# Performance work log

Measured on AMD Instinct MI355X. Metric: run time of the kernel, lower is better.

## Reference

```python
import jax, jax.numpy as jnp
import numpy as np

BOX_WARP = 1.0
RAY_START = 2.25
RAY_END = 3.3
S = 32  # depth_resolution (coarse), N_importance = 0


def bilinear_sample(image, coords):
    """Faithful port of the custom grid_sample (align_corners=True mapping).
    image: [B, C, H, W]; coords: [B, M, 2] in [-1, 1]. Returns [B, M, C]."""
    B, C, H, W = image.shape
    ix = (coords[..., 0] + 1.0) * 0.5 * (W - 1)
    iy = (coords[..., 1] + 1.0) * 0.5 * (H - 1)
    ix0 = jnp.floor(ix)
    iy0 = jnp.floor(iy)
    ix1 = ix0 + 1.0
    iy1 = iy0 + 1.0
    # weights use UNclamped corner positions, matching the torch code
    w_nw = (ix1 - ix) * (iy1 - iy)
    w_ne = (ix - ix0) * (iy1 - iy)
    w_sw = (ix1 - ix) * (iy - iy0)
    w_se = (ix - ix0) * (iy - iy0)
    ix0c = jnp.clip(ix0, 0, W - 1).astype(jnp.int32)
    ix1c = jnp.clip(ix1, 0, W - 1).astype(jnp.int32)
    iy0c = jnp.clip(iy0, 0, H - 1).astype(jnp.int32)
    iy1c = jnp.clip(iy1, 0, H - 1).astype(jnp.int32)
    img = image.reshape(B, C, H * W)

    def gather(iyc, ixc):
        idx = iyc * W + ixc  # [B, M]
        return jnp.take_along_axis(img, idx[:, None, :], axis=2)  # [B, C, M]

    out = (gather(iy0c, ix0c) * w_nw[:, None, :]
           + gather(iy0c, ix1c) * w_ne[:, None, :]
           + gather(iy1c, ix0c) * w_sw[:, None, :]
           + gather(iy1c, ix1c) * w_se[:, None, :])
    return out.transpose(0, 2, 1)  # [B, M, C]


def setup_inputs() -> dict:
    key = jax.random.key(0)
    k1, k2, k3, k4, k5 = jax.random.split(key, 5)
    N, n_planes, C, H, W = 2, 3, 32, 256, 256
    R = 16384
    vol_planes = jax.random.normal(k1, (N, n_planes, C, H, W), dtype=jnp.float32)
    dirs = jax.random.normal(k2, (N, R, 3), dtype=jnp.float32)
    dirs = dirs / jnp.linalg.norm(dirs, axis=-1, keepdims=True)
    # camera on sphere of radius 2.7 looking through origin -> samples in box
    ray_origins = -2.7 * dirs
    w1 = jax.random.normal(k3, (C, 64), dtype=jnp.float32) * (1.0 / np.sqrt(C))
    b1 = jnp.zeros((64,), dtype=jnp.float32)
    w2 = jax.random.normal(k4, (64, 33), dtype=jnp.float32) * (1.0 / 8.0)
    b2 = jnp.zeros((33,), dtype=jnp.float32)
    return {"vol_planes": vol_planes, "ray_origins": ray_origins,
            "ray_directions": dirs, "w1": w1, "b1": b1, "w2": w2, "b2": b2}


def reference(vol_planes, ray_origins, ray_directions, w1, b1, w2, b2):
    N, n_planes, C, H, W = vol_planes.shape
    R = ray_origins.shape[1]
    # --- sample_stratified (deterministic: midpoint of each bin) ---
    t = (jnp.arange(S, dtype=vol_planes.dtype) + 0.5) / S
    d = RAY_START + (RAY_END - RAY_START) * t  # [S]
    depths = jnp.broadcast_to(d[None, None, :, None], (N, R, S, 1))
    coords = ray_origins[:, :, None, :] + depths * ray_directions[:, :, None, :]
    M = R * S
    coords = coords.reshape(N, M, 3) * (2.0 / BOX_WARP)
    # --- project_onto_planes (vol_proj=True): xyz, yzx, xzy; sampler uses xy ---
    xy = coords[..., jnp.array([0, 1])]
    yz = coords[..., jnp.array([1, 2])]
    xz = coords[..., jnp.array([0, 2])]
    proj = jnp.stack([xy, yz, xz], axis=1).reshape(N * n_planes, M, 2)
    feats = bilinear_sample(vol_planes.reshape(N * n_planes, C, H, W), proj)
    feats = feats.reshape(N, n_planes, M, C).mean(axis=1)  # aggregate planes
    # --- decoder: small MLP -> 1 sigma + 32 rgb features (EG3D style) ---
    h = jax.nn.softplus(feats @ w1 + b1)
    o = h @ w2 + b2
    sigma = o[..., :1].reshape(N, R, S, 1)
    rgb = (jax.nn.sigmoid(o[..., 1:]) * 1.002 - 0.001).reshape(N, R, S, 32)
    # --- MipRayMarcher2 ---
    deltas = depths[:, :, 1:] - depths[:, :, :-1]
    colors_mid = 0.5 * (rgb[:, :, :-1] + rgb[:, :, 1:])
    densities_mid = 0.5 * (sigma[:, :, :-1] + sigma[:, :, 1:])
    densities_mid = jax.nn.softplus(densities_mid - 1.0)
    alpha = 1.0 - jnp.exp(-deltas * densities_mid)  # [N,R,S-1,1]
    trans = jnp.cumprod(
        jnp.concatenate([jnp.ones_like(alpha[:, :, :1]), 1.0 - alpha + 1e-10],
                        axis=2), axis=2)[:, :, :-1]
    weights = alpha * trans
    rgb_final = (weights * colors_mid).sum(axis=2)  # [N, R, 32]
    return rgb_final
```

## Files before the change

### kernel.cpp

```cpp
#include <hip/hip_runtime.h>
#include <math.h>

#define HH 256
#define WW 256
#define CC 32
#define SS 32
#define NRAYS 32768
#define RPB 8

#define FXB_OFF 0
#define SIG_OFF 20480
#define WST_OFF 21504
#define W2T_OFF 25600
#define ALP_OFF 31744
#define POOLSZ  32768

typedef __attribute__((ext_vector_type(8))) short short8;
typedef __attribute__((ext_vector_type(4))) float f32x4;

__device__ __forceinline__ f32x4 mfma16(short8 a, short8 b, f32x4 c) {
    return __builtin_amdgcn_mfma_f32_16x16x32_bf16(a, b, c, 0, 0, 0);
}

__device__ __forceinline__ float bf2f(unsigned short u) {
    union { unsigned int ui; float f; } v; v.ui = ((unsigned int)u) << 16; return v.f;
}
__device__ __forceinline__ float lo2f(unsigned int w) {
    union { unsigned int ui; float f; } v; v.ui = w << 16; return v.f;
}
__device__ __forceinline__ float hi2f(unsigned int w) {
    union { unsigned int ui; float f; } v; v.ui = w & 0xffff0000u; return v.f;
}
__device__ __forceinline__ unsigned short f2bf(float f) {
    union { float f; unsigned int u; } v; v.f = f;
    unsigned int u = v.u;
    unsigned int r = u + 0x7fffu + ((u >> 16) & 1u);
    return (unsigned short)(r >> 16);
}
__device__ __forceinline__ unsigned int pk_bf16(float a, float b) {
    return (unsigned int)f2bf(a) | ((unsigned int)f2bf(b) << 16);
}
__device__ __forceinline__ int iclamp(int x, int lo, int hi) {
    return x < lo ? lo : (x > hi ? hi : x);
}
__device__ __forceinline__ float softplus_f(float z) {
    return fmaxf(z, 0.f) + log1pf(expf(-fabsf(z)));
}
__device__ __forceinline__ float softplus_fast(float z) {
    return fmaxf(z, 0.f) + __logf(1.0f + __expf(-fabsf(z)));
}
__device__ __forceinline__ float sigmoid_fast(float z) {
    return __builtin_amdgcn_rcpf(1.0f + __expf(-z));
}

template<bool F32>
__device__ __forceinline__ float ldv(const void* p, size_t i) {
    if (F32) return ((const float*)p)[i];
    else     return bf2f(((const unsigned short*)p)[i]);
}

__device__ __forceinline__ int compute_flag(const void* rayo) {
    const float* f = (const float*)rayo;
    const unsigned short* u = (const unsigned short*)rayo;
    float sf = 0.f, sb = 0.f;
    for (int r = 0; r < 8; r++) {
        const float a = f[3 * r], b = f[3 * r + 1], c = f[3 * r + 2];
        sf += fminf(fabsf(a * a + b * b + c * c - 7.29f), 1e3f);
        const float x = bf2f(u[3 * r]), y = bf2f(u[3 * r + 1]), z = bf2f(u[3 * r + 2]);
        sb += fminf(fabsf(x * x + y * y + z * z - 7.29f), 1e3f);
    }
    return (sf < sb) ? 1 : 0;
}

__global__ __launch_bounds__(1024) void transpose_tex(
    const void* __restrict__ vol, unsigned short* __restrict__ tex,
    const void* __restrict__ rayo) {
    __shared__ __align__(16) unsigned short tb[32][129];
    __shared__ int fsh;
    const int l = threadIdx.x;
    if (l == 0) fsh = compute_flag(rayo);
    __syncthreads();
    const int flag = fsh;

    const int tx = l & 31, ty = l >> 5;
    const int wq = l >> 3, cq = l & 7;
    const int w0 = blockIdx.x * 128;
    const int h  = blockIdx.y;
    const int img = blockIdx.z;
    const size_t srcE = (((size_t)img * CC + ty) * HH + h) * WW + w0 + 4 * tx;
    const size_t dstE = (((size_t)img * HH + h) * WW + (w0 + wq)) * CC + 4 * cq;
    if (flag) {
        const float4 v = *(const float4*)((const float*)vol + srcE);
        tb[ty][4 * tx + 0] = f2bf(v.x); tb[ty][4 * tx + 1] = f2bf(v.y);
        tb[ty][4 * tx + 2] = f2bf(v.z); tb[ty][4 * tx + 3] = f2bf(v.w);
    } else {
        *(ushort4*)&tb[ty][4 * tx] = *(const ushort4*)((const unsigned short*)vol + srcE);
    }
    __syncthreads();
    ushort4 o;
    o.x = tb[4 * cq + 0][wq]; o.y = tb[4 * cq + 1][wq];
    o.z = tb[4 * cq + 2][wq]; o.w = tb[4 * cq + 3][wq];
    *(ushort4*)(tex + dstE) = o;
}

template<bool F32>
__device__ void render_mfma_body(
    const unsigned short* __restrict__ tex,
    const void* __restrict__ rayo, const void* __restrict__ rayd,
    const void* __restrict__ w1b, const void* __restrict__ b1b,
    const void* __restrict__ w2b, const void* __restrict__ b2b,
    void* __restrict__ outp, char* __restrict__ pool)
{
    const int t = threadIdx.x;
    unsigned short* fxB = (unsigned short*)(pool + FXB_OFF);
    float* sigL = (float*)(pool + SIG_OFF);
    unsigned short* w1t = (unsigned short*)(pool + WST_OFF);
    unsigned short* w2t = (unsigned short*)(pool + W2T_OFF);
    float* aL = (float*)(pool + ALP_OFF);

    for (int i = t; i < 2048; i += 256) {
        const int n = i >> 5, k = i & 31;
        w1t[i] = f2bf(ldv<F32>(w1b, (size_t)k * 64 + n));
    }
    for (int i = t; i < 3072; i += 256) {
        const int n = i >> 6, k = i & 63;
        w2t[i] = (n < 33) ? f2bf(ldv<F32>(w2b, (size_t)k * 33 + n)) : (unsigned short)0;
    }
    __syncthreads();

    {
        const int rl = t >> 5;
        const int L  = t & 31;
        const int c4 = L & 7;
        const int sub = L >> 3;
        const int gray = blockIdx.x * RPB + rl;
        const int n = gray >> 14;
        const size_t rb = (size_t)gray * 3;
        const float ox = ldv<F32>(rayo, rb), oy = ldv<F32>(rayo, rb + 1), oz = ldv<F32>(rayo, rb + 2);
        const float dx = ldv<F32>(rayd, rb), dy = ldv<F32>(rayd, rb + 1), dz = ldv<F32>(rayd, rb + 2);
        const char* texb = (const char*)tex;
        const unsigned int cb = (unsigned int)c4 * 8;

        #pragma unroll 2
        for (int k = 0; k < 8; ++k) {
            const int s = sub * 8 + k;
            const float d = 2.25f + 1.05f * ((s + 0.5f) * (1.0f / 32.0f));
            const float x = (ox + d * dx) * 2.0f;
            const float y = (oy + d * dy) * 2.0f;
            const float z = (oz + d * dz) * 2.0f;
            float a0[4] = {0.f, 0.f, 0.f, 0.f};
            float a1[4] = {0.f, 0.f, 0.f, 0.f};
            float a2[4] = {0.f, 0.f, 0.f, 0.f};
            #pragma unroll
            for (int p = 0; p < 3; p++) {
                const float u = (p == 0) ? x : ((p == 1) ? y : x);
                const float v = (p == 0) ? y : z;
                const float ixf = fmaf(u, 127.5f, 127.5f);
                const float iyf = fmaf(v, 127.5f, 127.5f);
                const float ix0f = floorf(ixf), iy0f = floorf(iyf);
                const float wx1 = ixf - ix0f, wy1 = iyf - iy0f;
                const float wx0 = 1.f - wx1,  wy0 = 1.f - wy1;
                const int ix0 = iclamp((int)ix0f, 0, 255);
                const int ix1 = iclamp((int)ix0f + 1, 0, 255);
                const int iy0 = iclamp((int)iy0f, 0, 255);
                const int iy1 = iclamp((int)iy0f + 1, 0, 255);
                const float w00 = wx0 * wy0, w01 = wx1 * wy0, w10 = wx0 * wy1, w11 = wx1 * wy1;
                const unsigned int pb = (unsigned int)(n * 3 + p) * (HH * WW * CC * 2) + cb;
                const uint2 q00 = *(const uint2*)(texb + pb + ((unsigned int)(iy0 * WW + ix0) << 6));
                const uint2 q01 = *(const uint2*)(texb + pb + ((unsigned int)(iy0 * WW + ix1) << 6));
                const uint2 q10 = *(const uint2*)(texb + pb + ((unsigned int)(iy1 * WW + ix0) << 6));
                const uint2 q11 = *(const uint2*)(texb + pb + ((unsigned int)(iy1 * WW + ix1) << 6));
                const float v00[4] = { lo2f(q00.x), hi2f(q00.x), lo2f(q00.y), hi2f(q00.y) };
                const float v01[4] = { lo2f(q01.x), hi2f(q01.x), lo2f(q01.y), hi2f(q01.y) };
                const float v10[4] = { lo2f(q10.x), hi2f(q10.x), lo2f(q10.y), hi2f(q10.y) };
                const float v11[4] = { lo2f(q11.x), hi2f(q11.x), lo2f(q11.y), hi2f(q11.y) };
                #pragma unroll
                for (int i = 0; i < 4; i++) {
                    float acc = w00 * v00[i];
                    acc = fmaf(w01, v01[i], acc);
                    acc = fmaf(w10, v10[i], acc);
                    acc = fmaf(w11, v11[i], acc);
                    if (p == 0) a0[i] = acc; else if (p == 1) a1[i] = acc; else a2[i] = acc;
                }
            }
            uint2 pk;
            pk.x = pk_bf16((a0[0] + a1[0] + a2[0]) * (1.0f / 3.0f),
                           (a0[1] + a1[1] + a2[1]) * (1.0f / 3.0f));
            pk.y = pk_bf16((a0[2] + a1[2] + a2[2]) * (1.0f / 3.0f),
                           (a0[3] + a1[3] + a2[3]) * (1.0f / 3.0f));
            *(uint2*)(pool + FXB_OFF + (rl * 32 + s) * 80 + c4 * 8) = pk;
        }
    }

    const int w = t >> 6;
    const int lane = t & 63;
    const int l16 = lane & 15, quad = lane >> 4;

    short8 b1f[4];
    #pragma unroll
    for (int nt = 0; nt < 4; nt++)
        b1f[nt] = *(const short8*)(pool + WST_OFF + (nt * 16 + l16) * 64 + quad * 16);
    short8 b2f[3][2];
    #pragma unroll
    for (int nt = 0; nt < 3; nt++)
        #pragma unroll
        for (int ks = 0; ks < 2; ks++)
            b2f[nt][ks] = *(const short8*)(pool + W2T_OFF + (nt * 16 + l16) * 128 + ks * 64 + quad * 16);
    float bb1[4], bb2[3];
    #pragma unroll
    for (int nt = 0; nt < 4; nt++) bb1[nt] = ldv<F32>(b1b, nt * 16 + l16);
    #pragma unroll
    for (int nt = 0; nt < 3; nt++) {
        const int n2 = nt * 16 + l16;
        bb2[nt] = (n2 < 33) ? ldv<F32>(b2b, n2) : 0.f;
    }
    __syncthreads();

    {
        char* hb = pool + WST_OFF + w * 2304;
        #pragma unroll 1
        for (int mt = 0; mt < 4; mt++) {
            const int rbase = w * 64 + mt * 16;
            const short8 a1 = *(const short8*)(pool + FXB_OFF + (rbase + l16) * 80 + quad * 16);
            #pragma unroll
            for (int nt = 0; nt < 4; nt++) {
                f32x4 hc = { bb1[nt], bb1[nt], bb1[nt], bb1[nt] };
                hc = mfma16(a1, b1f[nt], hc);
                #pragma unroll
                for (int r = 0; r < 4; r++) {
                    const float hv = softplus_fast(hc[r]);
                    *(unsigned short*)(hb + (quad * 4 + r) * 144 + (nt * 16 + l16) * 2) = f2bf(hv);
                }
            }
            const short8 a2k0 = *(const short8*)(hb + l16 * 144 + quad * 16);
            const short8 a2k1 = *(const short8*)(hb + l16 * 144 + 64 + quad * 16);
            #pragma unroll
            for (int nt = 0; nt < 3; nt++) {
                f32x4 o = { bb2[nt], bb2[nt], bb2[nt], bb2[nt] };
                o = mfma16(a2k0, b2f[nt][0], o);
                o = mfma16(a2k1, b2f[nt][1], o);
                #pragma unroll
                for (int r = 0; r < 4; r++) {
                    const int row = rbase + quad * 4 + r;
                    if (nt == 0) {
                        if (l16 == 0) sigL[row] = o[r];
                        else fxB[row * 40 + (l16 - 1)] =
                                 f2bf(fmaf(sigmoid_fast(o[r]), 1.002f, -0.001f));
                    } else if (nt == 1) {
                        fxB[row * 40 + (15 + l16)] =
                                 f2bf(fmaf(sigmoid_fast(o[r]), 1.002f, -0.001f));
                    } else if (l16 == 0) {
                        fxB[row * 40 + 31] =
                                 f2bf(fmaf(sigmoid_fast(o[r]), 1.002f, -0.001f));
                    }
                }
            }
        }
    }
    __syncthreads();

    {
        const int rl = t >> 5, sm = t & 31;
        if (sm < 31) {
            const float sp = sigL[rl * 32 + sm];
            const float sn = sigL[rl * 32 + sm + 1];
            const float m = 0.5f * (sp + sn) - 1.0f;
            const float dens = fmaxf(m, 0.f) + __logf(1.0f + __expf(-fabsf(m)));
            aL[rl * 32 + sm] = 1.0f - __expf(-(1.05f / 32.0f) * dens);
        }
    }
    __syncthreads();

    {
        const int rl = t >> 5, sm = t & 31;
        if (sm == 0) {
            float T = 1.0f;
            #pragma unroll
            for (int j = 0; j < 31; j++) {
                const float a = aL[rl * 32 + j];
                aL[rl * 32 + j] = (a * T) * 0.5f;
                T *= (1.0f - a + 1e-10f);
            }
        }
    }
    __syncthreads();

    {
        const int rl = t >> 5, c = t & 31;
        const int gr2 = blockIdx.x * RPB + rl;
        float acc = 0.0f;
        float rp = bf2f(fxB[(rl * 32 + 0) * 40 + c]);
        #pragma unroll 4
        for (int sm = 0; sm < 31; sm++) {
            const float rn = bf2f(fxB[(rl * 32 + sm + 1) * 40 + c]);
            acc = fmaf(aL[rl * 32 + sm], rp + rn, acc);
            rp = rn;
        }
        const size_t oidx = (size_t)gr2 * 32 + c;
        if (F32) ((float*)outp)[oidx] = acc;
        else     ((unsigned short*)outp)[oidx] = f2bf(acc);
    }
}

__global__ __launch_bounds__(256, 4) void render_fast(
    const unsigned short* __restrict__ tex, const void* __restrict__ rayo,
    const void* __restrict__ rayd, const void* __restrict__ w1b,
    const void* __restrict__ b1b, const void* __restrict__ w2b,
    const void* __restrict__ b2b, void* __restrict__ outp)
{
    __shared__ __align__(16) char pool[POOLSZ];
    int* fsh = (int*)(pool + ALP_OFF);
    if (threadIdx.x == 0) *fsh = compute_flag(rayo);
    __syncthreads();
    const int flag = *fsh;
    if (flag) render_mfma_body<true >(tex, rayo, rayd, w1b, b1b, w2b, b2b, outp, pool);
    else      render_mfma_body<false>(tex, rayo, rayd, w1b, b1b, w2b, b2b, outp, pool);
}

template<bool F32>
__device__ __forceinline__ void render_body(
    const void* __restrict__ vol, const void* __restrict__ rayo,
    const void* __restrict__ rayd, const void* __restrict__ w1b,
    const void* __restrict__ b1b, const void* __restrict__ w2b,
    const void* __restrict__ b2b, void* __restrict__ outp,
    float* wsm, float (*rgbL)[SS][33], float (*sigL)[SS])
{
    const int t = threadIdx.x;
    for (int i = t; i < 4257; i += 256) {
        float v;
        if (i < 2048)       v = ldv<F32>(w1b, i);
        else if (i < 2112)  v = ldv<F32>(b1b, i - 2048);
        else if (i < 4224)  v = ldv<F32>(w2b, i - 2112);
        else                v = ldv<F32>(b2b, i - 4224);
        wsm[i] = v;
    }
    __syncthreads();

    const int rl = t >> 5;
    const int s  = t & 31;
    const int gray = blockIdx.x * RPB + rl;
    const int n = gray >> 14;

    const size_t rbase = (size_t)gray * 3;
    const float ox = ldv<F32>(rayo, rbase), oy = ldv<F32>(rayo, rbase + 1), oz = ldv<F32>(rayo, rbase + 2);
    const float dx = ldv<F32>(rayd, rbase), dy = ldv<F32>(rayd, rbase + 1), dz = ldv<F32>(rayd, rbase + 2);
    const float d = 2.25f + 1.05f * ((s + 0.5f) * (1.0f / 32.0f));
    const float x = (ox + d * dx) * 2.0f;
    const float y = (oy + d * dy) * 2.0f;
    const float z = (oz + d * dz) * 2.0f;

    float fx[32];
    #pragma unroll
    for (int c = 0; c < 32; c++) fx[c] = 0.f;

    #pragma unroll
    for (int p = 0; p < 3; p++) {
        const float u = (p == 0) ? x : ((p == 1) ? y : x);
        const float v = (p == 0) ? y : z;
        const float ixf = fmaf(u, 127.5f, 127.5f);
        const float iyf = fmaf(v, 127.5f, 127.5f);
        const float ix0f = floorf(ixf), iy0f = floorf(iyf);
        const float wx1 = ixf - ix0f, wy1 = iyf - iy0f;
        const float wx0 = 1.f - wx1,  wy0 = 1.f - wy1;
        const int ix0 = iclamp((int)ix0f, 0, 255);
        const int ix1 = iclamp((int)ix0f + 1, 0, 255);
        const int iy0 = iclamp((int)iy0f, 0, 255);
        const int iy1 = iclamp((int)iy0f + 1, 0, 255);
        const float wnw = wx0 * wy0, wne = wx1 * wy0, wsw = wx0 * wy1, wse = wx1 * wy1;
        const int i00 = iy0 * WW + ix0, i01 = iy0 * WW + ix1;
        const int i10 = iy1 * WW + ix0, i11 = iy1 * WW + ix1;
        const size_t pb = (size_t)(n * 3 + p) * CC * HH * WW;
        #pragma unroll
        for (int c = 0; c < 32; c++) {
            const size_t cb = pb + (size_t)c * (HH * WW);
            fx[c] += wnw * ldv<F32>(vol, cb + i00) + wne * ldv<F32>(vol, cb + i01)
                   + wsw * ldv<F32>(vol, cb + i10) + wse * ldv<F32>(vol, cb + i11);
        }
    }
    #pragma unroll
    for (int c = 0; c < 32; c++) fx[c] *= (1.0f / 3.0f);

    const float* W1 = wsm;
    const float* B1 = wsm + 2048;
    const float* W2 = wsm + 2112;
    const float* B2 = wsm + 4224;

    float h[64];
    #pragma unroll
    for (int j = 0; j < 64; j++) h[j] = B1[j];
    #pragma unroll
    for (int c = 0; c < 32; c++) {
        const float f = fx[c];
        #pragma unroll
        for (int j = 0; j < 64; j++) h[j] = fmaf(f, W1[c * 64 + j], h[j]);
    }
    #pragma unroll
    for (int j = 0; j < 64; j++) h[j] = softplus_f(h[j]);

    #pragma unroll 1
    for (int k = 0; k < 33; k++) {
        float zz = B2[k];
        #pragma unroll
        for (int j = 0; j < 64; j++) zz = fmaf(h[j], W2[j * 33 + k], zz);
        if (k == 0) sigL[rl][s] = zz;
        else {
            const float sg = 1.0f / (1.0f + expf(-zz));
            rgbL[rl][s][k - 1] = fmaf(sg, 1.002f, -0.001f);
        }
    }
    __syncthreads();

    const int c = t & 31;
    const float delta = 1.05f / 32.0f;
    float T = 1.0f, acc = 0.0f;
    float sig_prev = sigL[rl][0];
    float rgb_prev = rgbL[rl][0][c];
    #pragma unroll 1
    for (int sm = 0; sm < 31; sm++) {
        const float sig_next = sigL[rl][sm + 1];
        const float rgb_next = rgbL[rl][sm + 1][c];
        const float dens = softplus_f(0.5f * (sig_prev + sig_next) - 1.0f);
        const float alpha = 1.0f - expf(-delta * dens);
        acc += alpha * T * 0.5f * (rgb_prev + rgb_next);
        T *= (1.0f - alpha + 1e-10f);
        sig_prev = sig_next;
        rgb_prev = rgb_next;
    }
    const size_t oidx = (size_t)gray * 32 + c;
    if (F32) ((float*)outp)[oidx] = acc;
    else     ((unsigned short*)outp)[oidx] = f2bf(acc);
}

__global__ __launch_bounds__(256) void render_any(
    const void* __restrict__ vol, const void* __restrict__ rayo,
    const void* __restrict__ rayd, const void* __restrict__ w1b,
    const void* __restrict__ b1b, const void* __restrict__ w2b,
    const void* __restrict__ b2b, void* __restrict__ outp)
{
    __shared__ float wsm[4257];
    __shared__ float rgbL[RPB][SS][33];
    __shared__ float sigL[RPB][SS];
    __shared__ int fsh;
    if (threadIdx.x == 0) fsh = compute_flag(rayo);
    __syncthreads();
    const int flag = fsh;
    if (flag) render_body<true >(vol, rayo, rayd, w1b, b1b, w2b, b2b, outp, wsm, rgbL, sigL);
    else      render_body<false>(vol, rayo, rayd, w1b, b1b, w2b, b2b, outp, wsm, rgbL, sigL);
}

extern "C" void kernel_launch(void* const* d_in, const int* in_sizes, int n_in,
                              void* d_out, int out_size, void* d_ws, size_t ws_size,
                              hipStream_t stream) {
    const void* vol  = d_in[0];
    const void* rayo = d_in[1];
    const void* rayd = d_in[2];
    const void* w1   = d_in[3];
    const void* b1   = d_in[4];
    const void* w2   = d_in[5];
    const void* b2   = d_in[6];
    unsigned short* tex = (unsigned short*)d_ws;

    const size_t need = (size_t)6 * HH * WW * CC * 2;

    if (ws_size >= need) {
        transpose_tex<<<dim3(WW / 128, HH, 6), dim3(1024), 0, stream>>>(vol, tex, rayo);
        render_fast<<<dim3(NRAYS / RPB), dim3(256), 0, stream>>>(
            tex, rayo, rayd, w1, b1, w2, b2, d_out);
    } else {
        render_any<<<dim3(NRAYS / RPB), dim3(256), 0, stream>>>(
            vol, rayo, rayd, w1, b1, w2, b2, d_out);
    }
}
```

Before: 242.3 us.

## Fuse texture transpose and render into one cooperative persistent kernel

Replaces the two-kernel sequence (transpose to channel-last bf16 texture, then render) with one cooperative kernel of 1024 blocks. Each block transposes three 128-wide rows, performs a grid-wide sync, then renders four ray chunks persistently while keeping the MLP weight fragments in registers. This removes a kernel launch boundary and amortises weight staging across chunks. In exchange it adds a grid barrier, less parallel slack (1024 blocks instead of 4096), and relies on all blocks fitting co-resident, falling back to the old path if the cooperative launch fails.

Measured after the change: 413.0 us. 70.4% more time.

```diff
diff --git a/kernel.cpp b/kernel.cpp
--- a/kernel.cpp
+++ b/kernel.cpp
@@ -1,5 +1,8 @@
 #include <hip/hip_runtime.h>
+#include <hip/hip_cooperative_groups.h>
 #include <math.h>
+
+namespace cg = cooperative_groups;
 
 #define HH 256
 #define WW 256
@@ -72,68 +75,41 @@
     return (sf < sb) ? 1 : 0;
 }
 
-__global__ __launch_bounds__(1024) void transpose_tex(
-    const void* __restrict__ vol, unsigned short* __restrict__ tex,
-    const void* __restrict__ rayo) {
-    __shared__ __align__(16) unsigned short tb[32][129];
-    __shared__ int fsh;
-    const int l = threadIdx.x;
-    if (l == 0) fsh = compute_flag(rayo);
-    __syncthreads();
-    const int flag = fsh;
-
-    const int tx = l & 31, ty = l >> 5;
-    const int wq = l >> 3, cq = l & 7;
-    const int w0 = blockIdx.x * 128;
-    const int h  = blockIdx.y;
-    const int img = blockIdx.z;
-    const size_t srcE = (((size_t)img * CC + ty) * HH + h) * WW + w0 + 4 * tx;
-    const size_t dstE = (((size_t)img * HH + h) * WW + (w0 + wq)) * CC + 4 * cq;
-    if (flag) {
-        const float4 v = *(const float4*)((const float*)vol + srcE);
-        tb[ty][4 * tx + 0] = f2bf(v.x); tb[ty][4 * tx + 1] = f2bf(v.y);
-        tb[ty][4 * tx + 2] = f2bf(v.z); tb[ty][4 * tx + 3] = f2bf(v.w);
-    } else {
-        *(ushort4*)&tb[ty][4 * tx] = *(const ushort4*)((const unsigned short*)vol + srcE);
-    }
-    __syncthreads();
-    ushort4 o;
-    o.x = tb[4 * cq + 0][wq]; o.y = tb[4 * cq + 1][wq];
-    o.z = tb[4 * cq + 2][wq]; o.w = tb[4 * cq + 3][wq];
-    *(ushort4*)(tex + dstE) = o;
-}
-
 template<bool F32>
-__device__ void render_mfma_body(
-    const unsigned short* __restrict__ tex,
+__device__ __forceinline__ void stage_weights(
+    const void* __restrict__ w1b, const void* __restrict__ w2b, char* pool) {
+    const int t = threadIdx.x;
+    unsigned short* w1t = (unsigned short*)(pool + WST_OFF);
+    unsigned short* w2t = (unsigned short*)(pool + W2T_OFF);
+    for (int i = t; i < 2048; i += 256) {
+        const int n = i >> 5, k = i & 31;
+        w1t[i] = f2bf(ldv<F32>(w1b, (size_t)k * 64 + n));
+    }
+    for (int i = t; i < 3072; i += 256) {
+        const int n = i >> 6, k = i & 63;
+        w2t[i] = (n < 33) ? f2bf(ldv<F32>(w2b, (size_t)k * 33 + n)) : (unsigned short)0;
+    }
+}
+
+template<bool F32>
+__device__ __forceinline__ void render_chunk(
+    int B,
+    const unsigned short* tex,
     const void* __restrict__ rayo, const void* __restrict__ rayd,
-    const void* __restrict__ w1b, const void* __restrict__ b1b,
-    const void* __restrict__ w2b, const void* __restrict__ b2b,
-    void* __restrict__ outp, char* __restrict__ pool)
+    void* __restrict__ outp, char* pool,
+    const short8* b1f, const short8 (*b2f)[2], const float* bb1, const float* bb2)
 {
     const int t = threadIdx.x;
     unsigned short* fxB = (unsigned short*)(pool + FXB_OFF);
     float* sigL = (float*)(pool + SIG_OFF);
-    unsigned short* w1t = (unsigned short*)(pool + WST_OFF);
-    unsigned short* w2t = (unsigned short*)(pool + W2T_OFF);
     float* aL = (float*)(pool + ALP_OFF);
-
-    for (int i = t; i < 2048; i += 256) {
-        const int n = i >> 5, k = i & 31;
-        w1t[i] = f2bf(ldv<F32>(w1b, (size_t)k * 64 + n));
-    }
-    for (int i = t; i < 3072; i += 256) {
-        const int n = i >> 6, k = i & 63;
-        w2t[i] = (n < 33) ? f2bf(ldv<F32>(w2b, (size_t)k * 33 + n)) : (unsigned short)0;
-    }
-    __syncthreads();
 
     {
         const int rl = t >> 5;
         const int L  = t & 31;
         const int c4 = L & 7;
         const int sub = L >> 3;
-        const int gray = blockIdx.x * RPB + rl;
+        const int gray = B * RPB + rl;
         const int n = gray >> 14;
         const size_t rb = (size_t)gray * 3;
         const float ox = ldv<F32>(rayo, rb), oy = ldv<F32>(rayo, rb + 1), oz = ldv<F32>(rayo, rb + 2);
@@ -191,32 +167,12 @@
             *(uint2*)(pool + FXB_OFF + (rl * 32 + s) * 80 + c4 * 8) = pk;
         }
     }
-
-    const int w = t >> 6;
-    const int lane = t & 63;
-    const int l16 = lane & 15, quad = lane >> 4;
-
-    short8 b1f[4];
-    #pragma unroll
-    for (int nt = 0; nt < 4; nt++)
-        b1f[nt] = *(const short8*)(pool + WST_OFF + (nt * 16 + l16) * 64 + quad * 16);
-    short8 b2f[3][2];
-    #pragma unroll
-    for (int nt = 0; nt < 3; nt++)
-        #pragma unroll
-        for (int ks = 0; ks < 2; ks++)
-            b2f[nt][ks] = *(const short8*)(pool + W2T_OFF + (nt * 16 + l16) * 128 + ks * 64 + quad * 16);
-    float bb1[4], bb2[3];
-    #pragma unroll
-    for (int nt = 0; nt < 4; nt++) bb1[nt] = ldv<F32>(b1b, nt * 16 + l16);
-    #pragma unroll
-    for (int nt = 0; nt < 3; nt++) {
-        const int n2 = nt * 16 + l16;
-        bb2[nt] = (n2 < 33) ? ldv<F32>(b2b, n2) : 0.f;
-    }
     __syncthreads();
 
     {
+        const int w = t >> 6;
+        const int lane = t & 63;
+        const int l16 = lane & 15, quad = lane >> 4;
         char* hb = pool + WST_OFF + w * 2304;
         #pragma unroll 1
         for (int mt = 0; mt < 4; mt++) {
@@ -287,7 +243,7 @@
 
     {
         const int rl = t >> 5, c = t & 31;
-        const int gr2 = blockIdx.x * RPB + rl;
+        const int gr2 = B * RPB + rl;
         float acc = 0.0f;
         float rp = bf2f(fxB[(rl * 32 + 0) * 40 + c]);
         #pragma unroll 4
@@ -302,6 +258,164 @@
     }
 }
 
+template<bool F32>
+__device__ void fused_body(
+    const void* __restrict__ vol, unsigned short* tex,
+    const void* __restrict__ rayo, const void* __restrict__ rayd,
+    const void* __restrict__ w1b, const void* __restrict__ b1b,
+    const void* __restrict__ w2b, const void* __restrict__ b2b,
+    void* __restrict__ outp, char* pool)
+{
+    const int t = threadIdx.x;
+
+    stage_weights<F32>(w1b, w2b, pool);
+
+    unsigned short* tb = (unsigned short*)(pool + FXB_OFF);
+    #pragma unroll 1
+    for (int j = 0; j < 3; j++) {
+        const int T = blockIdx.x * 3 + j;
+        const int w0 = (T & 1) * 128;
+        const int h  = (T >> 1) & 255;
+        const int img = T >> 9;
+        __syncthreads();
+        #pragma unroll
+        for (int it = 0; it < 4; it++) {
+            const int ty = (t >> 5) + 8 * it;
+            const int tx = t & 31;
+            const size_t srcE = (((size_t)img * CC + ty) * HH + h) * WW + w0 + 4 * tx;
+            if (F32) {
+                const float4 v = *(const float4*)((const float*)vol + srcE);
+                tb[ty * 129 + 4 * tx + 0] = f2bf(v.x); tb[ty * 129 + 4 * tx + 1] = f2bf(v.y);
+                tb[ty * 129 + 4 * tx + 2] = f2bf(v.z); tb[ty * 129 + 4 * tx + 3] = f2bf(v.w);
+            } else {
+                *(ushort4*)&tb[ty * 129 + 4 * tx] =
+                    *(const ushort4*)((const unsigned short*)vol + srcE);
+            }
+        }
+        __syncthreads();
+        #pragma unroll
+        for (int it = 0; it < 4; it++) {
+            const int wq = (t >> 3) + 32 * it;
+            const int cq = t & 7;
+            const size_t dstE = (((size_t)img * HH + h) * WW + (w0 + wq)) * CC + 4 * cq;
+            ushort4 o;
+            o.x = tb[(4 * cq + 0) * 129 + wq]; o.y = tb[(4 * cq + 1) * 129 + wq];
+            o.z = tb[(4 * cq + 2) * 129 + wq]; o.w = tb[(4 * cq + 3) * 129 + wq];
+            *(ushort4*)(tex + dstE) = o;
+        }
+    }
+    __syncthreads();
+
+    const int lane = t & 63;
+    const int l16 = lane & 15, quad = lane >> 4;
+    short8 b1f[4];
+    #pragma unroll
+    for (int nt = 0; nt < 4; nt++)
+        b1f[nt] = *(const short8*)(pool + WST_OFF + (nt * 16 + l16) * 64 + quad * 16);
+    short8 b2f[3][2];
+    #pragma unroll
+    for (int nt = 0; nt < 3; nt++)
+        #pragma unroll
+        for (int ks = 0; ks < 2; ks++)
+            b2f[nt][ks] = *(const short8*)(pool + W2T_OFF + (nt * 16 + l16) * 128 + ks * 64 + quad * 16);
+    float bb1[4], bb2[3];
+    #pragma unroll
+    for (int nt = 0; nt < 4; nt++) bb1[nt] = ldv<F32>(b1b, nt * 16 + l16);
+    #pragma unroll
+    for (int nt = 0; nt < 3; nt++) {
+        const int n2 = nt * 16 + l16;
+        bb2[nt] = (n2 < 33) ? ldv<F32>(b2b, n2) : 0.f;
+    }
+
+    cg::this_grid().sync();
+
+    #pragma unroll 1
+    for (int ch = 0; ch < 4; ch++) {
+        render_chunk<F32>(blockIdx.x + 1024 * ch, tex, rayo, rayd, outp, pool,
+                          b1f, b2f, bb1, bb2);
+        __syncthreads();
+    }
+}
+
+__global__ __launch_bounds__(256, 4) void fused_all(
+    const void* vol, unsigned short* tex,
+    const void* rayo, const void* rayd,
+    const void* w1b, const void* b1b, const void* w2b, const void* b2b,
+    void* outp)
+{
+    __shared__ __align__(16) char pool[POOLSZ];
+    int* fsh = (int*)(pool + ALP_OFF);
+    if (threadIdx.x == 0) *fsh = compute_flag(rayo);
+    __syncthreads();
+    const int flag = *fsh;
+    if (flag) fused_body<true >(vol, tex, rayo, rayd, w1b, b1b, w2b, b2b, outp, pool);
+    else      fused_body<false>(vol, tex, rayo, rayd, w1b, b1b, w2b, b2b, outp, pool);
+}
+
+__global__ __launch_bounds__(1024) void transpose_tex(
+    const void* __restrict__ vol, unsigned short* __restrict__ tex,
+    const void* __restrict__ rayo) {
+    __shared__ __align__(16) unsigned short tb[32][129];
+    __shared__ int fsh;
+    const int l = threadIdx.x;
+    if (l == 0) fsh = compute_flag(rayo);
+    __syncthreads();
+    const int flag = fsh;
+    const int tx = l & 31, ty = l >> 5;
+    const int wq = l >> 3, cq = l & 7;
+    const int w0 = blockIdx.x * 128;
+    const int h  = blockIdx.y;
+    const int img = blockIdx.z;
+    const size_t srcE = (((size_t)img * CC + ty) * HH + h) * WW + w0 + 4 * tx;
+    const size_t dstE = (((size_t)img * HH + h) * WW + (w0 + wq)) * CC + 4 * cq;
+    if (flag) {
+        const float4 v = *(const float4*)((const float*)vol + srcE);
+        tb[ty][4 * tx + 0] = f2bf(v.x); tb[ty][4 * tx + 1] = f2bf(v.y);
+        tb[ty][4 * tx + 2] = f2bf(v.z); tb[ty][4 * tx + 3] = f2bf(v.w);
+    } else {
+        *(ushort4*)&tb[ty][4 * tx] = *(const ushort4*)((const unsigned short*)vol + srcE);
+    }
+    __syncthreads();
+    ushort4 o;
+    o.x = tb[4 * cq + 0][wq]; o.y = tb[4 * cq + 1][wq];
+    o.z = tb[4 * cq + 2][wq]; o.w = tb[4 * cq + 3][wq];
+    *(ushort4*)(tex + dstE) = o;
+}
+
+template<bool F32>
+__device__ void render_fast_body(
+    const unsigned short* __restrict__ tex,
+    const void* __restrict__ rayo, const void* __restrict__ rayd,
+    const void* __restrict__ w1b, const void* __restrict__ b1b,
+    const void* __restrict__ w2b, const void* __restrict__ b2b,
+    void* __restrict__ outp, char* pool)
+{
+    const int t = threadIdx.x;
+    stage_weights<F32>(w1b, w2b, pool);
+    __syncthreads();
+    const int lane = t & 63;
+    const int l16 = lane & 15, quad = lane >> 4;
+    short8 b1f[4];
+    #pragma unroll
+    for (int nt = 0; nt < 4; nt++)
+        b1f[nt] = *(const short8*)(pool + WST_OFF + (nt * 16 + l16) * 64 + quad * 16);
+    short8 b2f[3][2];
+    #pragma unroll
+    for (int nt = 0; nt < 3; nt++)
+        #pragma unroll
+        for (int ks = 0; ks < 2; ks++)
+            b2f[nt][ks] = *(const short8*)(pool + W2T_OFF + (nt * 16 + l16) * 128 + ks * 64 + quad * 16);
+    float bb1[4], bb2[3];
+    #pragma unroll
+    for (int nt = 0; nt < 4; nt++) bb1[nt] = ldv<F32>(b1b, nt * 16 + l16);
+    #pragma unroll
+    for (int nt = 0; nt < 3; nt++) {
+        const int n2 = nt * 16 + l16;
+        bb2[nt] = (n2 < 33) ? ldv<F32>(b2b, n2) : 0.f;
+    }
+    render_chunk<F32>(blockIdx.x, tex, rayo, rayd, outp, pool, b1f, b2f, bb1, bb2);
+}
+
 __global__ __launch_bounds__(256, 4) void render_fast(
     const unsigned short* __restrict__ tex, const void* __restrict__ rayo,
     const void* __restrict__ rayd, const void* __restrict__ w1b,
@@ -313,8 +427,8 @@
     if (threadIdx.x == 0) *fsh = compute_flag(rayo);
     __syncthreads();
     const int flag = *fsh;
-    if (flag) render_mfma_body<true >(tex, rayo, rayd, w1b, b1b, w2b, b2b, outp, pool);
-    else      render_mfma_body<false>(tex, rayo, rayd, w1b, b1b, w2b, b2b, outp, pool);
+    if (flag) render_fast_body<true >(tex, rayo, rayd, w1b, b1b, w2b, b2b, outp, pool);
+    else      render_fast_body<false>(tex, rayo, rayd, w1b, b1b, w2b, b2b, outp, pool);
 }
 
 template<bool F32>
@@ -463,9 +577,16 @@
     const size_t need = (size_t)6 * HH * WW * CC * 2;
 
     if (ws_size >= need) {
-        transpose_tex<<<dim3(WW / 128, HH, 6), dim3(1024), 0, stream>>>(vol, tex, rayo);
-        render_fast<<<dim3(NRAYS / RPB), dim3(256), 0, stream>>>(
-            tex, rayo, rayd, w1, b1, w2, b2, d_out);
+        void* args[9] = { (void*)&vol, (void*)&tex, (void*)&rayo, (void*)&rayd,
+                          (void*)&w1, (void*)&b1, (void*)&w2, (void*)&b2,
+                          (void*)&d_out };
+        hipError_t e = hipLaunchCooperativeKernel(
+            (const void*)fused_all, dim3(1024), dim3(256), args, 0, stream);
+        if (e != hipSuccess) {
+            transpose_tex<<<dim3(WW / 128, HH, 6), dim3(1024), 0, stream>>>(vol, tex, rayo);
+            render_fast<<<dim3(NRAYS / RPB), dim3(256), 0, stream>>>(
+                tex, rayo, rayd, w1, b1, w2, b2, d_out);
+        }
     } else {
         render_any<<<dim3(NRAYS / RPB), dim3(256), 0, stream>>>(
             vol, rayo, rayd, w1, b1, w2, b2, d_out);
```
